# Kernel tuning notes

Measured on AMD Instinct MI355X. Metric: run time of the kernel, lower is better.

## Reference

```python
import jax, jax.numpy as jnp
import numpy as np
import math

# dims: batch, in-channels, freq bins, frames(=cropsize), ffn dim, bands
B, C, BINS, W, FF, NB = 16, 8, 1024, 256, 2048, 4
EPS = 1e-5


def _ln(x, g, b):
    m = x.mean(-1, keepdims=True)
    v = ((x - m) ** 2).mean(-1, keepdims=True)
    return (x - m) / jnp.sqrt(v + EPS) * g + b


def _conv1d(x, w, groups=1):
    # x: [b, Cin, L], w: [Cout, Cin//groups, K], 'same' padding
    pad = (w.shape[-1] - 1) // 2
    return jax.lax.conv_general_dilated(
        x, w, (1,), [(pad, pad)],
        dimension_numbers=('NCH', 'OIH', 'NCH'), feature_group_count=groups)


def _mb_attn(x, mem, qw, qb, kw, kb, vw, vb, ow, ob, er, dist_w):
    # MultibandFrameAttention with skewed relative-position bias
    b, w, c = x.shape
    d = c // NB
    q = (x @ qw.T + qb).reshape(b, w, NB, d).transpose(0, 2, 1, 3)    # [b,nb,w,d]
    k = (mem @ kw.T + kb).reshape(b, w, NB, d).transpose(0, 2, 3, 1)  # [b,nb,d,w]
    v = (mem @ vw.T + vb).reshape(b, w, NB, d).transpose(0, 2, 1, 3)  # [b,nb,w,d]
    # skew trick: q @ er -> pad left on last dim -> transpose -> drop first row
    qer = jnp.einsum('bnwd,dc->bnwc', q, er)                           # [b,nb,w,W]
    skew = jnp.pad(qer, ((0, 0), (0, 0), (0, 0), (1, 0)))
    skew = skew.transpose(0, 1, 3, 2)[:, :, 1:, :]                     # [b,nb,W,w]
    idx = jnp.arange(w)
    dist = jnp.abs(idx[:, None] - idx[None, :]).astype(x.dtype) / 2.0  # [w,w]
    p = dist[None] * dist_w + skew                                     # [b,nb,w,w]
    qk = jnp.einsum('bnwd,bndk->bnwk', q, k) / math.sqrt(c)
    a = jax.nn.softmax(qk + p, axis=-1)
    o = jnp.einsum('bnwk,bnkd->bnwd', a, v).transpose(0, 2, 1, 3).reshape(b, w, c)
    return o @ ow.T + ob


def setup_inputs() -> dict:
    key = jax.random.key(0)
    ks = jax.random.split(key, 24)
    rn = lambda k, s, sc=0.02: jax.random.normal(k, s, dtype=jnp.float32) * sc
    d = BINS // NB
    ones = lambda n: jnp.ones((n,), jnp.float32)
    zeros = lambda n: jnp.zeros((n,), jnp.float32)
    return {
        'x': jax.random.normal(ks[0], (B, C, BINS, W), jnp.float32),
        'bott_w': rn(ks[1], (1, C), 0.3),
        'bn_g': ones(1), 'bn_b': zeros(1), 'bn_m': zeros(1), 'bn_v': ones(1),
        'glu_w': rn(ks[2], (2 * BINS, BINS)),
        'n1g': ones(BINS), 'n1b': zeros(BINS),
        'c1L_w': rn(ks[3], (2 * FF, BINS)),
        'c1R_w': rn(ks[4], (FF // 2, BINS, 3)),
        'n2g': ones(2 * FF), 'n2b': zeros(2 * FF),
        'c2dw_w': rn(ks[5], (2 * FF, 1, 9), 0.1),
        'c2pw_w': rn(ks[6], (FF // 2, 2 * FF)),
        'n3g': ones(BINS), 'n3b': zeros(BINS),
        'qw': rn(ks[7], (BINS, BINS)), 'qb': zeros(BINS),
        'kw': rn(ks[8], (BINS, BINS)), 'kb': zeros(BINS),
        'vw': rn(ks[9], (BINS, BINS)), 'vb': zeros(BINS),
        'ow': rn(ks[10], (BINS, BINS)), 'ob': zeros(BINS),
        'er': rn(ks[11], (d, W), 0.02),
        'dist_w': rn(ks[12], (NB, W, 1), 0.02),
        'n4g': ones(BINS), 'n4b': zeros(BINS),
        'c3_w': rn(ks[13], (2 * FF, BINS)),
        'c4_w': rn(ks[14], (BINS, 2 * FF)),
        'n5g': ones(BINS), 'n5b': zeros(BINS),
    }


def reference(x, bott_w, bn_g, bn_b, bn_m, bn_v, glu_w, n1g, n1b,
              c1L_w, c1R_w, n2g, n2b, c2dw_w, c2pw_w, n3g, n3b,
              qw, qb, kw, kb, vw, vb, ow, ob, er, dist_w,
              n4g, n4b, c3_w, c4_w, n5g, n5b):
    # bottleneck: Linear(C->1) over channel dim, BatchNorm2d(1) eval, ReLU
    h0 = jnp.einsum('bchw,oc->bohw', x, bott_w)                        # [b,1,bins,w]
    h0 = (h0 - bn_m[None, :, None, None]) / jnp.sqrt(bn_v[None, :, None, None] + EPS)
    h0 = jax.nn.relu(h0 * bn_g[None, :, None, None] + bn_b[None, :, None, None])
    xs = h0[:, 0].transpose(0, 2, 1)                                   # [b,w,bins]

    # GLU block
    g = xs @ glu_w.T
    a, bgate = g[..., :BINS], g[..., BINS:]
    xs = _ln(xs + a * jax.nn.sigmoid(bgate), n1g, n1b)

    # conv/linear FFN
    hL = jax.nn.relu(xs @ c1L_w.T)                                     # [b,w,2ff]
    hR = jax.nn.relu(_conv1d(xs.transpose(0, 2, 1), c1R_w).transpose(0, 2, 1))
    hR = jnp.pad(hR, ((0, 0), (0, 0), (0, hL.shape[2] - hR.shape[2])))
    h = _ln(hL + hR, n2g, n2b)
    t = _conv1d(h.transpose(0, 2, 1), c2dw_w, groups=2 * FF)           # depthwise
    t = jnp.einsum('bcl,oc->bol', t, c2pw_w).transpose(0, 2, 1)        # [b,w,ff//2]
    t = jnp.pad(t, ((0, 0), (0, 0), (0, xs.shape[2] - t.shape[2])))
    xs = _ln(xs + t, n3g, n3b)

    # multiband attention (self)
    h = _mb_attn(xs, xs, qw, qb, kw, kb, vw, vb, ow, ob, er, dist_w)
    xs = _ln(xs + h, n4g, n4b)

    # final FFN
    h = jax.nn.relu(xs @ c3_w.T) @ c4_w.T
    xs = _ln(xs + h, n5g, n5b)
    return xs.transpose(0, 2, 1)[:, None]                              # [b,1,bins,w]
```

## Files before the change

### kernel.cpp

```cpp
#include <hip/hip_runtime.h>
#include <hip/hip_bf16.h>

#define EPSF 1e-5f

typedef unsigned short u16;
typedef unsigned int   u32;
typedef __attribute__((ext_vector_type(8))) short bf16x8;
typedef __attribute__((ext_vector_type(4))) float f32x4;

#define SWZ(row) (((row) & 7) << 3)

__device__ __forceinline__ u16 f2bf(float f) {
    u32 u = __builtin_bit_cast(u32, f);
    u32 r = u + 0x7fffu + ((u >> 16) & 1u);
    return (u16)(r >> 16);
}
__device__ __forceinline__ float bf2f(u16 h) {
    return __builtin_bit_cast(float, (u32)h << 16);
}
__device__ __forceinline__ float4 bf4f(ushort4 v) {
    return make_float4(bf2f(v.x), bf2f(v.y), bf2f(v.z), bf2f(v.w));
}
__device__ __forceinline__ ushort4 f4bf(float a, float b, float c, float d) {
    ushort4 o; o.x = f2bf(a); o.y = f2bf(b); o.z = f2bf(c); o.w = f2bf(d); return o;
}
__device__ __forceinline__ void gld16(void* lds, const void* gsrc) {
    __builtin_amdgcn_global_load_lds(
        (const __attribute__((address_space(1))) u32*)gsrc,
        (__attribute__((address_space(3))) u32*)lds, 16, 0, 0);
}

__device__ __forceinline__ float wred_sum(float v) {
#pragma unroll
    for (int off = 32; off; off >>= 1) v += __shfl_xor(v, off, 64);
    return v;
}
__device__ __forceinline__ void block_red2(float& s1, float& s2, int tid) {
    __shared__ float red[8];
    s1 = wred_sum(s1); s2 = wred_sum(s2);
    const int lane = tid & 63, wid = tid >> 6;
    if (!lane) { red[wid] = s1; red[4 + wid] = s2; }
    __syncthreads();
    s1 = red[0] + red[1] + red[2] + red[3];
    s2 = red[4] + red[5] + red[6] + red[7];
}

struct SetupArgs {
    const float* ws[9]; u16* wd[9]; int wn[9];
    const float* c1r; u16* c1rd;
    const float* er;  u16* erd;
    const float* dw;  float* dwd;
    const float* qb;  const float* kb; const float* vb; float* bcat;
    u16* zp;
    int off[15];
};
__global__ __launch_bounds__(256)
void setup_k(SetupArgs a)
{
    const int b = blockIdx.x;
    int seg = 0;
    while (seg < 13 && b >= a.off[seg + 1]) ++seg;
    const int i = (b - a.off[seg]) * 256 + threadIdx.x;
    if (seg < 9) {
        if (i < a.wn[seg]) {
            const float4 v = ((const float4*)a.ws[seg])[i];
            const float s = (seg == 6) ? 0.03125f : 1.f;
            ((ushort4*)a.wd[seg])[i] = f4bf(v.x * s, v.y * s, v.z * s, v.w * s);
        }
    } else if (seg == 9) {
        if (i < 3145728) {
            const int q = i / 3072, rem = i - q * 3072;
            const int ks = rem >> 10, ci = rem & 1023;
            a.c1rd[i] = f2bf(a.c1r[((long)q * 1024 + ci) * 3 + ks]);
        }
    } else if (seg == 10) {
        if (i < 65536) { const int c = i >> 8, d = i & 255; a.erd[i] = f2bf(a.er[d * 256 + c]); }
    } else if (seg == 11) {
        if (i < 36864) { const int k = i >> 12, c = i & 4095; a.dwd[i] = a.dw[c * 9 + k]; }
    } else if (seg == 12) {
        if (i < 3072) {
            const float* s = (i < 1024) ? a.qb : ((i < 2048) ? a.kb : a.vb);
            float v = s[i & 1023];
            if (i >= 1024 && i < 2048) v *= 0.03125f;
            a.bcat[i] = v;
        }
    } else {
        if (i < 8192) a.zp[i] = 0;
    }
}

__global__ __launch_bounds__(256)
void bottleneck_k(const float* __restrict__ x, const float* __restrict__ bw,
                  const float* __restrict__ bn_g, const float* __restrict__ bn_b,
                  const float* __restrict__ bn_m, const float* __restrict__ bn_v,
                  u16* __restrict__ xsb)
{
    __shared__ float tile[32][33];
    const int b = blockIdx.z, h0 = blockIdx.y * 32, w0 = blockIdx.x * 32;
    const int tid = threadIdx.x;
    const int tw = tid & 7, th = tid >> 3;
    float wreg[8];
#pragma unroll
    for (int ch = 0; ch < 8; ++ch) wreg[ch] = bw[ch];
    const float sc = bn_g[0] * rsqrtf(bn_v[0] + EPSF);
    const float sh = bn_b[0] - bn_m[0] * sc;
    float4 acc = make_float4(0.f, 0.f, 0.f, 0.f);
#pragma unroll
    for (int ch = 0; ch < 8; ++ch) {
        const float4 v = *(const float4*)&x[(((long)b * 8 + ch) * 1024 + h0 + th) * 256 + w0 + tw * 4];
        acc.x += v.x * wreg[ch]; acc.y += v.y * wreg[ch];
        acc.z += v.z * wreg[ch]; acc.w += v.w * wreg[ch];
    }
    tile[th][tw * 4 + 0] = fmaxf(acc.x * sc + sh, 0.f);
    tile[th][tw * 4 + 1] = fmaxf(acc.y * sc + sh, 0.f);
    tile[th][tw * 4 + 2] = fmaxf(acc.z * sc + sh, 0.f);
    tile[th][tw * 4 + 3] = fmaxf(acc.w * sc + sh, 0.f);
    __syncthreads();
    const int c = tid & 31, r = tid >> 5;
#pragma unroll
    for (int it = 0; it < 4; ++it) {
        const int wl = r + it * 8;
        xsb[((long)b * 256 + w0 + wl) * 1024 + h0 + c] = f2bf(tile[c][wl]);
    }
}

template<int ACT, int OUTBF, int BIAS, int SPLITK, int VOUT>
__global__ __launch_bounds__(512, 2)
void gemm8_k(const u16* __restrict__ A, const u16* __restrict__ B,
             const float* __restrict__ bias, void* __restrict__ Cout,
             int N, int K , int lda, int ldb, long partStride,
             u16* __restrict__ Vtp)
{
    extern __shared__ u16 lds[];
    const int m0 = blockIdx.y * 256, n0 = blockIdx.x * 256;
    const int koff = (SPLITK > 1) ? blockIdx.z * K : 0;
    const int nt = K >> 6;
    const int tid = threadIdx.x;
    const int lane = tid & 63, wid = tid >> 6;
    const int wr = ((wid >> 2) & 1) * 128;
    const int wc = (wid & 3) * 64;
    const int l15 = lane & 15, l4 = lane >> 4;

    const u16* Ag = A + (long)m0 * lda + koff;
    const u16* Bg = B + (long)n0 * ldb + koff;

    auto stage = [&](const u16* g, int ld, int ldsbase, int kcol, int h) {
#pragma unroll
        for (int is = 0; is < 2; ++is) {
            const int r = h * 128 + is * 64 + (tid >> 3);
            const int sc = ((tid & 7) * 8) ^ SWZ(r);
            gld16(&lds[ldsbase + h * 8192 + is * 4096 + tid * 8],
                  g + (long)r * ld + kcol + sc);
        }
    };
    auto frag = [&](int base, int row, int col) -> bf16x8 {
        return *(const bf16x8*)&lds[base + row * 64 + (col ^ SWZ(row))];
    };

    f32x4 acc[8][4] = {};

    stage(Ag, lda, 0, 0, 0);
    stage(Ag, lda, 0, 0, 1);
    stage(Bg, ldb, 32768, 0, 0);
    stage(Bg, ldb, 32768, 0, 1);
    if (nt > 1) {
        stage(Bg, ldb, 49152, 64, 0);
        stage(Bg, ldb, 49152, 64, 1);
        stage(Ag, lda, 16384, 64, 0);
        asm volatile("s_waitcnt vmcnt(6)" ::: "memory");
    } else {
        asm volatile("s_waitcnt vmcnt(0)" ::: "memory");
    }
    __builtin_amdgcn_s_barrier();

    for (int kt = 0; kt < nt; ++kt) {
        const int cs = kt & 1;
        const int ab = cs * 16384;
        const int bb = 32768 + cs * 16384;
        const int abn = (cs ^ 1) * 16384;
        const int kc1 = (kt + 1) * 64, kc2 = (kt + 2) * 64;
        bf16x8 alo[4][2], ahi[4][2], b01[2][2], b23[2][2];

#pragma unroll
        for (int i = 0; i < 4; ++i)
#pragma unroll
            for (int kk = 0; kk < 2; ++kk)
                alo[i][kk] = frag(ab, wr + i * 16 + l15, kk * 32 + l4 * 8);
#pragma unroll
        for (int j = 0; j < 2; ++j)
#pragma unroll
            for (int kk = 0; kk < 2; ++kk)
                b01[j][kk] = frag(bb, wc + j * 16 + l15, kk * 32 + l4 * 8);
        if (kt + 1 < nt) stage(Ag, lda, abn, kc1, 1);
        __builtin_amdgcn_s_barrier();
        asm volatile("s_waitcnt lgkmcnt(0)" ::: "memory");
        __builtin_amdgcn_s_setprio(1);
#pragma unroll
        for (int i = 0; i < 4; ++i)
#pragma unroll
            for (int j = 0; j < 2; ++j)
#pragma unroll
                for (int kk = 0; kk < 2; ++kk)
                    acc[i][j] = __builtin_amdgcn_mfma_f32_16x16x32_bf16(alo[i][kk], b01[j][kk], acc[i][j], 0, 0, 0);
        __builtin_amdgcn_s_setprio(0);
        __builtin_amdgcn_s_barrier();

#pragma unroll
        for (int j = 0; j < 2; ++j)
#pragma unroll
            for (int kk = 0; kk < 2; ++kk)
                b23[j][kk] = frag(bb, wc + (j + 2) * 16 + l15, kk * 32 + l4 * 8);
        if (kt + 2 < nt) stage(Bg, ldb, bb, kc2, 0);
        __builtin_amdgcn_s_barrier();
        asm volatile("s_waitcnt lgkmcnt(0)" ::: "memory");
        __builtin_amdgcn_s_setprio(1);
#pragma unroll
        for (int i = 0; i < 4; ++i)
#pragma unroll
            for (int j = 0; j < 2; ++j)
#pragma unroll
                for (int kk = 0; kk < 2; ++kk)
                    acc[i][j + 2] = __builtin_amdgcn_mfma_f32_16x16x32_bf16(alo[i][kk], b23[j][kk], acc[i][j + 2], 0, 0, 0);
        __builtin_amdgcn_s_setprio(0);
        __builtin_amdgcn_s_barrier();

#pragma unroll
        for (int i = 0; i < 4; ++i)
#pragma unroll
            for (int kk = 0; kk < 2; ++kk)
                ahi[i][kk] = frag(ab, wr + (i + 4) * 16 + l15, kk * 32 + l4 * 8);
        if (kt + 2 < nt) stage(Bg, ldb, bb, kc2, 1);
        __builtin_amdgcn_s_barrier();
        asm volatile("s_waitcnt lgkmcnt(0)" ::: "memory");
        __builtin_amdgcn_s_setprio(1);
#pragma unroll
        for (int i = 0; i < 4; ++i)
#pragma unroll
            for (int j = 0; j < 2; ++j)
#pragma unroll
                for (int kk = 0; kk < 2; ++kk)
                    acc[i + 4][j + 2] = __builtin_amdgcn_mfma_f32_16x16x32_bf16(ahi[i][kk], b23[j][kk], acc[i + 4][j + 2], 0, 0, 0);
        __builtin_amdgcn_s_setprio(0);
        __builtin_amdgcn_s_barrier();

        if (kt + 2 < nt) stage(Ag, lda, ab, kc2, 0);
        __builtin_amdgcn_s_barrier();
        __builtin_amdgcn_s_setprio(1);
#pragma unroll
        for (int i = 0; i < 4; ++i)
#pragma unroll
            for (int j = 0; j < 2; ++j)
#pragma unroll
                for (int kk = 0; kk < 2; ++kk)
                    acc[i + 4][j] = __builtin_amdgcn_mfma_f32_16x16x32_bf16(ahi[i][kk], b01[j][kk], acc[i + 4][j], 0, 0, 0);
        __builtin_amdgcn_s_setprio(0);
        if (kt + 2 < nt) {
            asm volatile("s_waitcnt vmcnt(6)" ::: "memory");
        } else {
            asm volatile("s_waitcnt vmcnt(0)" ::: "memory");
        }
        __builtin_amdgcn_s_barrier();
    }

    if (VOUT && n0 >= 2048) {
        const int zb4 = (m0 >> 8) * 4;
#pragma unroll
        for (int i = 0; i < 8; ++i)
#pragma unroll
            for (int j = 0; j < 4; ++j) {
                const int n = n0 + wc + j * 16 + l15;
                const int d = n - 2048, zn = d >> 8, dl = d & 255;
                const float bv = BIAS ? bias[n] : 0.f;
                const int w = wr + i * 16 + l4 * 4;
                ushort4 st = f4bf(acc[i][j][0] + bv, acc[i][j][1] + bv,
                                  acc[i][j][2] + bv, acc[i][j][3] + bv);
                *(ushort4*)&Vtp[((long)(zb4 + zn) * 256 + dl) * 256 + w] = st;
            }
    } else if (SPLITK > 1) {
        u16* Cp = (u16*)Cout + (long)blockIdx.z * partStride;
#pragma unroll
        for (int i = 0; i < 8; ++i)
#pragma unroll
            for (int j = 0; j < 4; ++j) {
                const int n = n0 + wc + j * 16 + l15;
#pragma unroll
                for (int q = 0; q < 4; ++q) {
                    const int m = m0 + wr + i * 16 + l4 * 4 + q;
                    Cp[(long)m * N + n] = f2bf(acc[i][j][q]);
                }
            }
    } else {
        float* Cf = (float*)Cout;
        u16*   Cb = (u16*)Cout;
#pragma unroll
        for (int i = 0; i < 8; ++i)
#pragma unroll
            for (int j = 0; j < 4; ++j) {
                const int n = n0 + wc + j * 16 + l15;
                const float bv = BIAS ? bias[n] : 0.f;
#pragma unroll
                for (int q = 0; q < 4; ++q) {
                    const int m = m0 + wr + i * 16 + l4 * 4 + q;
                    float v = acc[i][j][q] + bv;
                    if (ACT) v = fmaxf(v, 0.f);
                    if (OUTBF) Cb[(long)m * N + n] = f2bf(v);
                    else       Cf[(long)m * N + n] = v;
                }
            }
    }
}

__global__ __launch_bounds__(512, 2)
void ffconv8_k(const u16* __restrict__ Xb, const u16* __restrict__ Wl,
               const u16* __restrict__ Wr, const u16* __restrict__ zp,
               u16* __restrict__ Hout, u16* __restrict__ Cp3)
{
    extern __shared__ u16 lds[];
    const int bx = blockIdx.x;
    const int m0 = blockIdx.y * 256;
    const bool conv = bx >= 16;
    const int tap  = conv ? ((bx - 16) >> 2) : 0;
    const int shift = conv ? (tap - 1) : 0;
    const int n0 = conv ? (((bx - 16) & 3) * 256) : (bx * 256);
    const u16* Bbase = conv ? (Wr + (long)n0 * 3072 + tap * 1024)
                            : (Wl + (long)n0 * 1024);
    const int ldb = conv ? 3072 : 1024;
    const int nt = 16;
    const int tid = threadIdx.x;
    const int lane = tid & 63, wid = tid >> 6;
    const int wr = ((wid >> 2) & 1) * 128;
    const int wc = (wid & 3) * 64;
    const int l15 = lane & 15, l4 = lane >> 4;

    auto stageA = [&](int ldsbase, int kcol, int h) {
#pragma unroll
        for (int is = 0; is < 2; ++is) {
            const int r = h * 128 + is * 64 + (tid >> 3);
            const int sc = ((tid & 7) * 8) ^ SWZ(r);
            const int t = m0 + r;
            const int wp = (t & 255) + shift;
            const u16* src = ((unsigned)wp < 256u)
                ? Xb + (long)(t + shift) * 1024 + kcol + sc
                : zp;
            gld16(&lds[ldsbase + h * 8192 + is * 4096 + tid * 8], src);
        }
    };
    auto stageB = [&](int ldsbase, int kcol, int h) {
#pragma unroll
        for (int is = 0; is < 2; ++is) {
            const int r = h * 128 + is * 64 + (tid >> 3);
            const int sc = ((tid & 7) * 8) ^ SWZ(r);
            gld16(&lds[ldsbase + h * 8192 + is * 4096 + tid * 8],
                  Bbase + (long)r * ldb + kcol + sc);
        }
    };
    auto frag = [&](int base, int row, int col) -> bf16x8 {
        return *(const bf16x8*)&lds[base + row * 64 + (col ^ SWZ(row))];
    };

    f32x4 acc[8][4] = {};

    stageA(0, 0, 0);
    stageA(0, 0, 1);
    stageB(32768, 0, 0);
    stageB(32768, 0, 1);
    stageB(49152, 64, 0);
    stageB(49152, 64, 1);
    stageA(16384, 64, 0);
    asm volatile("s_waitcnt vmcnt(6)" ::: "memory");
    __builtin_amdgcn_s_barrier();

    for (int kt = 0; kt < nt; ++kt) {
        const int cs = kt & 1;
        const int ab = cs * 16384;
        const int bb = 32768 + cs * 16384;
        const int abn = (cs ^ 1) * 16384;
        const int kc1 = (kt + 1) * 64, kc2 = (kt + 2) * 64;
        bf16x8 alo[4][2], ahi[4][2], b01[2][2], b23[2][2];

#pragma unroll
        for (int i = 0; i < 4; ++i)
#pragma unroll
            for (int kk = 0; kk < 2; ++kk)
                alo[i][kk] = frag(ab, wr + i * 16 + l15, kk * 32 + l4 * 8);
#pragma unroll
        for (int j = 0; j < 2; ++j)
#pragma unroll
            for (int kk = 0; kk < 2; ++kk)
                b01[j][kk] = frag(bb, wc + j * 16 + l15, kk * 32 + l4 * 8);
        if (kt + 1 < nt) stageA(abn, kc1, 1);
        __builtin_amdgcn_s_barrier();
        asm volatile("s_waitcnt lgkmcnt(0)" ::: "memory");
        __builtin_amdgcn_s_setprio(1);
#pragma unroll
        for (int i = 0; i < 4; ++i)
#pragma unroll
            for (int j = 0; j < 2; ++j)
#pragma unroll
                for (int kk = 0; kk < 2; ++kk)
                    acc[i][j] = __builtin_amdgcn_mfma_f32_16x16x32_bf16(alo[i][kk], b01[j][kk], acc[i][j], 0, 0, 0);
        __builtin_amdgcn_s_setprio(0);
        __builtin_amdgcn_s_barrier();

#pragma unroll
        for (int j = 0; j < 2; ++j)
#pragma unroll
            for (int kk = 0; kk < 2; ++kk)
                b23[j][kk] = frag(bb, wc + (j + 2) * 16 + l15, kk * 32 + l4 * 8);
        if (kt + 2 < nt) stageB(bb, kc2, 0);
        __builtin_amdgcn_s_barrier();
        asm volatile("s_waitcnt lgkmcnt(0)" ::: "memory");
        __builtin_amdgcn_s_setprio(1);
#pragma unroll
        for (int i = 0; i < 4; ++i)
#pragma unroll
            for (int j = 0; j < 2; ++j)
#pragma unroll
                for (int kk = 0; kk < 2; ++kk)
                    acc[i][j + 2] = __builtin_amdgcn_mfma_f32_16x16x32_bf16(alo[i][kk], b23[j][kk], acc[i][j + 2], 0, 0, 0);
        __builtin_amdgcn_s_setprio(0);
        __builtin_amdgcn_s_barrier();

#pragma unroll
        for (int i = 0; i < 4; ++i)
#pragma unroll
            for (int kk = 0; kk < 2; ++kk)
                ahi[i][kk] = frag(ab, wr + (i + 4) * 16 + l15, kk * 32 + l4 * 8);
        if (kt + 2 < nt) stageB(bb, kc2, 1);
        __builtin_amdgcn_s_barrier();
        asm volatile("s_waitcnt lgkmcnt(0)" ::: "memory");
        __builtin_amdgcn_s_setprio(1);
#pragma unroll
        for (int i = 0; i < 4; ++i)
#pragma unroll
            for (int j = 0; j < 2; ++j)
#pragma unroll
                for (int kk = 0; kk < 2; ++kk)
                    acc[i + 4][j + 2] = __builtin_amdgcn_mfma_f32_16x16x32_bf16(ahi[i][kk], b23[j][kk], acc[i + 4][j + 2], 0, 0, 0);
        __builtin_amdgcn_s_setprio(0);
        __builtin_amdgcn_s_barrier();

        if (kt + 2 < nt) stageA(ab, kc2, 0);
        __builtin_amdgcn_s_barrier();
        __builtin_amdgcn_s_setprio(1);
#pragma unroll
        for (int i = 0; i < 4; ++i)
#pragma unroll
            for (int j = 0; j < 2; ++j)
#pragma unroll
                for (int kk = 0; kk < 2; ++kk)
                    acc[i + 4][j] = __builtin_amdgcn_mfma_f32_16x16x32_bf16(ahi[i][kk], b01[j][kk], acc[i + 4][j], 0, 0, 0);
        __builtin_amdgcn_s_setprio(0);
        if (kt + 2 < nt) {
            asm volatile("s_waitcnt vmcnt(6)" ::: "memory");
        } else {
            asm volatile("s_waitcnt vmcnt(0)" ::: "memory");
        }
        __builtin_amdgcn_s_barrier();
    }

    if (conv) {
        u16* Cp = Cp3 + (long)tap * 4194304;
#pragma unroll
        for (int i = 0; i < 8; ++i)
#pragma unroll
            for (int j = 0; j < 4; ++j) {
                const int n = n0 + wc + j * 16 + l15;
#pragma unroll
                for (int q = 0; q < 4; ++q) {
                    const int m = m0 + wr + i * 16 + l4 * 4 + q;
                    Cp[(long)m * 1024 + n] = f2bf(acc[i][j][q]);
                }
            }
    } else {
#pragma unroll
        for (int i = 0; i < 8; ++i)
#pragma unroll
            for (int j = 0; j < 4; ++j) {
                const int n = n0 + wc + j * 16 + l15;
#pragma unroll
                for (int q = 0; q < 4; ++q) {
                    const int m = m0 + wr + i * 16 + l4 * 4 + q;
                    Hout[(long)m * 4096 + n] = f2bf(fmaxf(acc[i][j][q], 0.f));
                }
            }
    }
}

__global__ __launch_bounds__(256, 2)
void attn_fused_k(const u16* __restrict__ QKVb, const u16* __restrict__ erT,
                  const u16* __restrict__ Vt, const float* __restrict__ dwp,
                  u16* __restrict__ Oc)
{
    __shared__ __align__(16) u16 As[4096];
    __shared__ __align__(16) u16 Bs[16384];
    __shared__ __align__(16) u16 Pl[16384];
    __shared__ float redM[4][64];
    __shared__ float redS[4][64];
    const int z = blockIdx.y, zb = z >> 2, zn = z & 3;
    const int m0 = blockIdx.x * 64;
    const int tid = threadIdx.x;
    const int lane = tid & 63, wid = tid >> 6;
    const int l15 = lane & 15, l4 = lane >> 4;

    const u16* Qg = QKVb + (long)(zb * 256) * 3072 + zn * 256;
    const u16* Kg = Qg + 1024;

    auto stageA64 = [&](const u16* g, long ld) {
#pragma unroll
        for (int p = 0; p < 2; ++p) {
            const int e = p * 2048 + tid * 8;
            const int r = e >> 6, c = e & 63;
            const int sc = c ^ SWZ(r);
            gld16(&As[e], g + (long)r * ld + sc);
        }
    };
    auto stageB256 = [&](const u16* g, long ld) {
#pragma unroll
        for (int p = 0; p < 8; ++p) {
            const int e = p * 2048 + tid * 8;
            const int r = e >> 6, c = e & 63;
            const int sc = c ^ SWZ(r);
            gld16(&Bs[e], g + (long)r * ld + sc);
        }
    };
    auto fragA = [&](int i, int kk) -> bf16x8 {
        const int row = i * 16 + l15, col = kk * 32 + l4 * 8;
        return *(const bf16x8*)&As[row * 64 + (col ^ SWZ(row))];
    };
    auto fragB = [&](int j, int kk) -> bf16x8 {
        const int row = wid * 64 + j * 16 + l15, col = kk * 32 + l4 * 8;
        return *(const bf16x8*)&Bs[row * 64 + (col ^ SWZ(row))];
    };
    auto fragP = [&](int kc, int i, int kk) -> bf16x8 {
        const int row = i * 16 + l15, col = kk * 32 + l4 * 8;
        return *(const bf16x8*)&Pl[kc * 4096 + row * 64 + (col ^ SWZ(row))];
    };

    f32x4 acc1[4][4] = {};

    for (int kc = 0; kc < 8; ++kc) {
        __syncthreads();
        if (kc < 4) {
            stageA64(Qg + (long)m0 * 3072 + kc * 64, 3072);
            stageB256(Kg + kc * 64, 3072);
        } else {
            stageA64(erT + (long)m0 * 256 + (kc - 4) * 64, 256);
            stageB256(Qg + (kc - 4) * 64, 3072);
        }
        __syncthreads();
#pragma unroll
        for (int i = 0; i < 4; ++i) {
            const bf16x8 a0 = fragA(i, 0), a1 = fragA(i, 1);
#pragma unroll
            for (int j = 0; j < 4; ++j) {
                acc1[i][j] = __builtin_amdgcn_mfma_f32_16x16x32_bf16(a0, fragB(j, 0), acc1[i][j], 0, 0, 0);
                acc1[i][j] = __builtin_amdgcn_mfma_f32_16x16x32_bf16(a1, fragB(j, 1), acc1[i][j], 0, 0, 0);
            }
        }
    }

#pragma unroll
    for (int i = 0; i < 4; ++i)
#pragma unroll
        for (int q = 0; q < 4; ++q) {
            const int mg = m0 + i * 16 + l4 * 4 + q;
            const float dw = dwp[zn * 256 + mg];
#pragma unroll
            for (int j = 0; j < 4; ++j) {
                const int ng = wid * 64 + j * 16 + l15;
                acc1[i][j][q] += fabsf((float)(mg - ng)) * 0.5f * dw;
            }
        }

    float rmax[4][4], rsum[4][4];
#pragma unroll
    for (int i = 0; i < 4; ++i)
#pragma unroll
        for (int q = 0; q < 4; ++q) {
            float mv = fmaxf(fmaxf(acc1[i][0][q], acc1[i][1][q]),
                             fmaxf(acc1[i][2][q], acc1[i][3][q]));
#pragma unroll
            for (int off = 1; off <= 8; off <<= 1) mv = fmaxf(mv, __shfl_xor(mv, off, 64));
            rmax[i][q] = mv;
        }
    if (l15 == 0) {
#pragma unroll
        for (int i = 0; i < 4; ++i)
#pragma unroll
            for (int q = 0; q < 4; ++q)
                redM[wid][i * 16 + l4 * 4 + q] = rmax[i][q];
    }
    __syncthreads();
#pragma unroll
    for (int i = 0; i < 4; ++i)
#pragma unroll
        for (int q = 0; q < 4; ++q) {
            const int ml = i * 16 + l4 * 4 + q;
            rmax[i][q] = fmaxf(fmaxf(redM[0][ml], redM[1][ml]), fmaxf(redM[2][ml], redM[3][ml]));
        }
#pragma unroll
    for (int i = 0; i < 4; ++i)
#pragma unroll
        for (int q = 0; q < 4; ++q) {
            float sv = 0.f;
#pragma unroll
            for (int j = 0; j < 4; ++j) {
                const float e = __expf(acc1[i][j][q] - rmax[i][q]);
                acc1[i][j][q] = e;
                sv += e;
            }
#pragma unroll
            for (int off = 1; off <= 8; off <<= 1) sv += __shfl_xor(sv, off, 64);
            rsum[i][q] = sv;
        }
    if (l15 == 0) {
#pragma unroll
        for (int i = 0; i < 4; ++i)
#pragma unroll
            for (int q = 0; q < 4; ++q)
                redS[wid][i * 16 + l4 * 4 + q] = rsum[i][q];
    }
    __syncthreads();
#pragma unroll
    for (int i = 0; i < 4; ++i)
#pragma unroll
        for (int q = 0; q < 4; ++q) {
            const int ml = i * 16 + l4 * 4 + q;
            rsum[i][q] = redS[0][ml] + redS[1][ml] + redS[2][ml] + redS[3][ml];
        }
#pragma unroll
    for (int i = 0; i < 4; ++i)
#pragma unroll
        for (int q = 0; q < 4; ++q) {
            const float rinv = 1.f / rsum[i][q];
            const int ml = i * 16 + l4 * 4 + q;
#pragma unroll
            for (int j = 0; j < 4; ++j) {
                const int nc = j * 16 + l15;
                Pl[wid * 4096 + ml * 64 + (nc ^ SWZ(ml))] = f2bf(acc1[i][j][q] * rinv);
            }
        }
    __syncthreads();

    f32x4 accO[4][4] = {};
    for (int kc = 0; kc < 4; ++kc) {
        __syncthreads();
        stageB256(Vt + (long)(z * 256) * 256 + kc * 64, 256);
        __syncthreads();
#pragma unroll
        for (int i = 0; i < 4; ++i) {
            const bf16x8 a0 = fragP(kc, i, 0), a1 = fragP(kc, i, 1);
#pragma unroll
            for (int j = 0; j < 4; ++j) {
                accO[i][j] = __builtin_amdgcn_mfma_f32_16x16x32_bf16(a0, fragB(j, 0), accO[i][j], 0, 0, 0);
                accO[i][j] = __builtin_amdgcn_mfma_f32_16x16x32_bf16(a1, fragB(j, 1), accO[i][j], 0, 0, 0);
            }
        }
    }

#pragma unroll
    for (int i = 0; i < 4; ++i)
#pragma unroll
        for (int j = 0; j < 4; ++j) {
            const int d = wid * 64 + j * 16 + l15;
#pragma unroll
            for (int q = 0; q < 4; ++q) {
                const int mg = m0 + i * 16 + l4 * 4 + q;
                Oc[(long)(zb * 256 + mg) * 1024 + zn * 256 + d] = f2bf(accO[i][j][q]);
            }
        }
}

__global__ __launch_bounds__(256)
void glu_ln_k(const u16* __restrict__ xs0, const u16* __restrict__ g2,
              const float* __restrict__ gam, const float* __restrict__ bet,
              u16* __restrict__ outb)
{
    const int t = blockIdx.x, tid = threadIdx.x;
    const int f0 = tid * 4;
    const long PS = 8388608;
    const float4 xv = bf4f(*(const ushort4*)&xs0[(long)t * 1024 + f0]);
    const float4 a0 = bf4f(*(const ushort4*)&g2[(long)t * 2048 + f0]);
    const float4 g0 = bf4f(*(const ushort4*)&g2[(long)t * 2048 + 1024 + f0]);
    const float4 a1 = bf4f(*(const ushort4*)&g2[PS + (long)t * 2048 + f0]);
    const float4 g1 = bf4f(*(const ushort4*)&g2[PS + (long)t * 2048 + 1024 + f0]);
    const float ax = a0.x + a1.x, ay = a0.y + a1.y, az = a0.z + a1.z, aw = a0.w + a1.w;
    const float gx = g0.x + g1.x, gy = g0.y + g1.y, gz = g0.z + g1.z, gw = g0.w + g1.w;
    float vals[4];
    vals[0] = xv.x + ax / (1.f + expf(-gx));
    vals[1] = xv.y + ay / (1.f + expf(-gy));
    vals[2] = xv.z + az / (1.f + expf(-gz));
    vals[3] = xv.w + aw / (1.f + expf(-gw));
    float s1 = vals[0] + vals[1] + vals[2] + vals[3];
    float s2 = vals[0]*vals[0] + vals[1]*vals[1] + vals[2]*vals[2] + vals[3]*vals[3];
    block_red2(s1, s2, tid);
    const float mean = s1 * (1.f / 1024.f);
    const float var  = s2 * (1.f / 1024.f) - mean * mean;
    const float rstd = rsqrtf(var + EPSF);
    const float4 gm = *(const float4*)&gam[f0];
    const float4 bt = *(const float4*)&bet[f0];
    *(ushort4*)&outb[(long)t * 1024 + f0] = f4bf(
        (vals[0] - mean) * rstd * gm.x + bt.x,
        (vals[1] - mean) * rstd * gm.y + bt.y,
        (vals[2] - mean) * rstd * gm.z + bt.z,
        (vals[3] - mean) * rstd * gm.w + bt.w);
}

template<int P, int BIAS>
__global__ __launch_bounds__(256)
void add_ln1024_k(const u16* __restrict__ A, const u16* __restrict__ Bp,
                  const float* __restrict__ bias,
                  const float* __restrict__ gam, const float* __restrict__ bet,
                  u16* __restrict__ outb)
{
    const int t = blockIdx.x, tid = threadIdx.x;
    const int f0 = tid * 4;
    const long PS = 4194304;
    const float4 a = bf4f(*(const ushort4*)&A[(long)t * 1024 + f0]);
    float4 b = bf4f(*(const ushort4*)&Bp[(long)t * 1024 + f0]);
#pragma unroll
    for (int p = 1; p < P; ++p) {
        const float4 bp = bf4f(*(const ushort4*)&Bp[p * PS + (long)t * 1024 + f0]);
        b.x += bp.x; b.y += bp.y; b.z += bp.z; b.w += bp.w;
    }
    if (BIAS) {
        const float4 bb = *(const float4*)&bias[f0];
        b.x += bb.x; b.y += bb.y; b.z += bb.z; b.w += bb.w;
    }
    float vals[4] = {a.x + b.x, a.y + b.y, a.z + b.z, a.w + b.w};
    float s1 = vals[0] + vals[1] + vals[2] + vals[3];
    float s2 = vals[0]*vals[0] + vals[1]*vals[1] + vals[2]*vals[2] + vals[3]*vals[3];
    block_red2(s1, s2, tid);
    const float mean = s1 * (1.f / 1024.f);
    const float var  = s2 * (1.f / 1024.f) - mean * mean;
    const float rstd = rsqrtf(var + EPSF);
    const float4 gm = *(const float4*)&gam[f0];
    const float4 bt = *(const float4*)&bet[f0];
    *(ushort4*)&outb[(long)t * 1024 + f0] = f4bf(
        (vals[0] - mean) * rstd * gm.x + bt.x,
        (vals[1] - mean) * rstd * gm.y + bt.y,
        (vals[2] - mean) * rstd * gm.z + bt.z,
        (vals[3] - mean) * rstd * gm.w + bt.w);
}

__global__ __launch_bounds__(256)
void add_ln4096_k(const u16* __restrict__ A, const u16* __restrict__ Bp,
                  const float* __restrict__ gam, const float* __restrict__ bet,
                  u16* __restrict__ outb)
{
    const int t = blockIdx.x, tid = threadIdx.x;
    const long PS = 4194304;
    const int f0 = tid * 16;
    float vals[16];
    const bf16x8 a0 = *(const bf16x8*)&A[(long)t * 4096 + f0];
    const bf16x8 a1 = *(const bf16x8*)&A[(long)t * 4096 + f0 + 8];
#pragma unroll
    for (int e = 0; e < 8; ++e) { vals[e] = bf2f((u16)a0[e]); vals[8 + e] = bf2f((u16)a1[e]); }
    if (tid < 64) {
#pragma unroll
        for (int c = 0; c < 4; ++c) {
            const int fc = f0 + c * 4;
            const float4 b0 = bf4f(*(const ushort4*)&Bp[(long)t * 1024 + fc]);
            const float4 b1 = bf4f(*(const ushort4*)&Bp[PS + (long)t * 1024 + fc]);
            const float4 b2 = bf4f(*(const ushort4*)&Bp[2 * PS + (long)t * 1024 + fc]);
            vals[c*4+0] += fmaxf(b0.x + b1.x + b2.x, 0.f);
            vals[c*4+1] += fmaxf(b0.y + b1.y + b2.y, 0.f);
            vals[c*4+2] += fmaxf(b0.z + b1.z + b2.z, 0.f);
            vals[c*4+3] += fmaxf(b0.w + b1.w + b2.w, 0.f);
        }
    }
    float s1 = 0.f, s2 = 0.f;
#pragma unroll
    for (int e = 0; e < 16; ++e) { s1 += vals[e]; s2 += vals[e] * vals[e]; }
    block_red2(s1, s2, tid);
    const float mean = s1 * (1.f / 4096.f);
    const float var  = s2 * (1.f / 4096.f) - mean * mean;
    const float rstd = rsqrtf(var + EPSF);
#pragma unroll
    for (int c = 0; c < 4; ++c) {
        const int fc = f0 + c * 4;
        const float4 gm = *(const float4*)&gam[fc];
        const float4 bt = *(const float4*)&bet[fc];
        *(ushort4*)&outb[(long)t * 4096 + fc] = f4bf(
            (vals[c*4+0] - mean) * rstd * gm.x + bt.x,
            (vals[c*4+1] - mean) * rstd * gm.y + bt.y,
            (vals[c*4+2] - mean) * rstd * gm.z + bt.z,
            (vals[c*4+3] - mean) * rstd * gm.w + bt.w);
    }
}

__global__ __launch_bounds__(256)
void dwconv8_k(const u16* __restrict__ h, const float* __restrict__ wT,
               u16* __restrict__ out)
{
    const long idx = (long)blockIdx.x * 256 + threadIdx.x;
    const int cg = (int)(idx & 511);
    const int t  = (int)(idx >> 9);
    const int w  = t & 255;
    const int c0 = cg * 8;
    float acc[8] = {};
#pragma unroll
    for (int k = 0; k < 9; ++k) {
        const int wp = w + k - 4;
        if ((unsigned)wp < 256u) {
            const bf16x8 hv = *(const bf16x8*)&h[(long)(t + k - 4) * 4096 + c0];
            const float4 w0 = *(const float4*)&wT[k * 4096 + c0];
            const float4 w1 = *(const float4*)&wT[k * 4096 + c0 + 4];
            acc[0] += bf2f((u16)hv[0]) * w0.x;
            acc[1] += bf2f((u16)hv[1]) * w0.y;
            acc[2] += bf2f((u16)hv[2]) * w0.z;
            acc[3] += bf2f((u16)hv[3]) * w0.w;
            acc[4] += bf2f((u16)hv[4]) * w1.x;
            acc[5] += bf2f((u16)hv[5]) * w1.y;
            acc[6] += bf2f((u16)hv[6]) * w1.z;
            acc[7] += bf2f((u16)hv[7]) * w1.w;
        }
    }
    bf16x8 res;
#pragma unroll
    for (int j = 0; j < 8; ++j) res[j] = (short)f2bf(acc[j]);
    *(bf16x8*)&out[(long)t * 4096 + c0] = res;
}

__global__ __launch_bounds__(256)
void transpose_out_k(const u16* __restrict__ xs, float* __restrict__ out)
{
    __shared__ u16 tile[32][34];
    const int b = blockIdx.z, f0 = blockIdx.y * 32, w0 = blockIdx.x * 32;
    const int tid = threadIdx.x, c = tid & 31, r = tid >> 5;
#pragma unroll
    for (int it = 0; it < 4; ++it) {
        const int w = w0 + r + it * 8;
        tile[r + it * 8][c] = xs[((long)b * 256 + w) * 1024 + f0 + c];
    }
    __syncthreads();
#pragma unroll
    for (int it = 0; it < 4; ++it) {
        const int fl = r + it * 8;
        out[((long)b * 1024 + f0 + fl) * 256 + w0 + c] = bf2f(tile[c][fl]);
    }
}

extern "C" void kernel_launch(void* const* d_in, const int* in_sizes, int n_in,
                              void* d_out, int out_size, void* d_ws, size_t ws_size,
                              hipStream_t stream)
{
    const float* x      = (const float*)d_in[0];
    const float* bott_w = (const float*)d_in[1];
    const float* bn_g   = (const float*)d_in[2];
    const float* bn_b   = (const float*)d_in[3];
    const float* bn_m   = (const float*)d_in[4];
    const float* bn_v   = (const float*)d_in[5];
    const float* glu_w  = (const float*)d_in[6];
    const float* n1g    = (const float*)d_in[7];
    const float* n1b    = (const float*)d_in[8];
    const float* c1L_w  = (const float*)d_in[9];
    const float* c1R_w  = (const float*)d_in[10];
    const float* n2g    = (const float*)d_in[11];
    const float* n2b    = (const float*)d_in[12];
    const float* c2dw_w = (const float*)d_in[13];
    const float* c2pw_w = (const float*)d_in[14];
    const float* n3g    = (const float*)d_in[15];
    const float* n3b    = (const float*)d_in[16];
    const float* qw     = (const float*)d_in[17];
    const float* qb     = (const float*)d_in[18];
    const float* kw     = (const float*)d_in[19];
    const float* kb     = (const float*)d_in[20];
    const float* vw     = (const float*)d_in[21];
    const float* vb     = (const float*)d_in[22];
    const float* ow     = (const float*)d_in[23];
    const float* ob     = (const float*)d_in[24];
    const float* er     = (const float*)d_in[25];
    const float* dist_w = (const float*)d_in[26];
    const float* n4g    = (const float*)d_in[27];
    const float* n4b    = (const float*)d_in[28];
    const float* c3_w   = (const float*)d_in[29];
    const float* c4_w   = (const float*)d_in[30];
    const float* n5g    = (const float*)d_in[31];
    const float* n5b    = (const float*)d_in[32];
    float* out = (float*)d_out;

    char* Wb_ = (char*)d_ws;
    auto Bf = [&](size_t mib) { return (u16*)(Wb_ + (mib << 20)); };
    u16* XA   = Bf(0);
    u16* XB   = Bf(8);
    u16* H0b  = Bf(32);
    u16* Hglu = Bf(64);
    u16* C3p  = Bf(64);
    u16* P4   = Bf(64);
    u16* H1b  = Bf(128);
    u16* Hdw  = Bf(160);
    u16* QKVb = Bf(192);
    u16* Vt   = Bf(216);
    u16* S1b  = Bf(264);
    u16* wGLU = Bf(296); u16* wC1L = Bf(300); u16* wC1R = Bf(308);
    u16* wC2P = Bf(314); u16* wQKV = Bf(322); u16* wO   = Bf(328);
    u16* wC3  = Bf(330); u16* wC4  = Bf(338);
    u16* erT  = Bf(346);
    u16* zp   = (u16*)(Wb_ + (346u << 20) + 131072);
    float* wdwT = (float*)(Wb_ + (346u << 20) + 131072 + 16384);
    float* bQKV = (float*)(Wb_ + (346u << 20) + 131072 + 16384 + 147456);

    const dim3 blk(256);
    const dim3 blk8(512);
    const long PS1 = 4194304;
    const size_t SH8 = 131072;

    SetupArgs sa;
    sa.ws[0] = glu_w;  sa.wd[0] = wGLU;            sa.wn[0] = 524288;
    sa.ws[1] = c1L_w;  sa.wd[1] = wC1L;            sa.wn[1] = 1048576;
    sa.ws[2] = c2pw_w; sa.wd[2] = wC2P;            sa.wn[2] = 1048576;
    sa.ws[3] = c3_w;   sa.wd[3] = wC3;             sa.wn[3] = 1048576;
    sa.ws[4] = c4_w;   sa.wd[4] = wC4;             sa.wn[4] = 1048576;
    sa.ws[5] = qw;     sa.wd[5] = wQKV;            sa.wn[5] = 262144;
    sa.ws[6] = kw;     sa.wd[6] = wQKV + 1048576;  sa.wn[6] = 262144;
    sa.ws[7] = vw;     sa.wd[7] = wQKV + 2097152;  sa.wn[7] = 262144;
    sa.ws[8] = ow;     sa.wd[8] = wO;              sa.wn[8] = 262144;
    sa.c1r = c1R_w; sa.c1rd = wC1R;
    sa.er  = er;    sa.erd  = erT;
    sa.dw  = c2dw_w; sa.dwd = wdwT;
    sa.qb = qb; sa.kb = kb; sa.vb = vb; sa.bcat = bQKV;
    sa.zp = zp;
    {
        int bc[14] = {2048, 4096, 4096, 4096, 4096, 1024, 1024, 1024, 1024,
                      12288, 256, 144, 12, 32};
        int acc = 0;
        for (int s = 0; s < 14; ++s) { sa.off[s] = acc; acc += bc[s]; }
        sa.off[14] = acc;
        setup_k<<<dim3(acc), blk, 0, stream>>>(sa);
    }

    bottleneck_k<<<dim3(8, 32, 16), blk, 0, stream>>>(x, bott_w, bn_g, bn_b, bn_m, bn_v, XA);

    gemm8_k<0,0,0,2,0><<<dim3(8, 16, 2), blk8, SH8, stream>>>(XA, wGLU, nullptr, Hglu,
        2048, 512, 1024, 1024, (long)4096 * 2048, nullptr);

    glu_ln_k<<<dim3(4096), blk, 0, stream>>>(XA, Hglu, n1g, n1b, XB);

    ffconv8_k<<<dim3(28, 16), blk8, SH8, stream>>>(XB, wC1L, wC1R, zp, H0b, C3p);

    add_ln4096_k<<<dim3(4096), blk, 0, stream>>>(H0b, C3p, n2g, n2b, H1b);

    dwconv8_k<<<dim3(8192), blk, 0, stream>>>(H1b, wdwT, Hdw);

    gemm8_k<0,0,0,4,0><<<dim3(4, 16, 4), blk8, SH8, stream>>>(Hdw, wC2P, nullptr, P4,
        1024, 1024, 4096, 4096, PS1, nullptr);

    add_ln1024_k<4,0><<<dim3(4096), blk, 0, stream>>>(XB, P4, nullptr, n3g, n3b, XA);

    gemm8_k<0,1,1,1,1><<<dim3(12, 16, 1), blk8, SH8, stream>>>(XA, wQKV, bQKV, QKVb,
        3072, 1024, 1024, 1024, 0, Vt);

    attn_fused_k<<<dim3(4, 64), blk, 0, stream>>>(QKVb, erT, Vt, dist_w, S1b);

    gemm8_k<0,0,0,4,0><<<dim3(4, 16, 4), blk8, SH8, stream>>>(S1b, wO, nullptr, P4,
        1024, 256, 1024, 1024, PS1, nullptr);

    add_ln1024_k<4,1><<<dim3(4096), blk, 0, stream>>>(XA, P4, ob, n4g, n4b, XB);

    gemm8_k<1,1,0,1,0><<<dim3(16, 16, 1), blk8, SH8, stream>>>(XB, wC3, nullptr, H0b,
        4096, 1024, 1024, 1024, 0, nullptr);

    gemm8_k<0,0,0,4,0><<<dim3(4, 16, 4), blk8, SH8, stream>>>(H0b, wC4, nullptr, P4,
        1024, 1024, 4096, 4096, PS1, nullptr);

    add_ln1024_k<4,0><<<dim3(4096), blk, 0, stream>>>(XB, P4, nullptr, n5g, n5b, XA);

    transpose_out_k<<<dim3(8, 32, 16), blk, 0, stream>>>(XA, out);

    (void)in_sizes; (void)n_in; (void)out_size; (void)ws_size;
}
```

Measured before the change: 464.6 us.

## Accumulate all three conv taps in-kernel instead of split-K partials

The conv branch of the fused FFN GEMM kernel now loops over all three taps inside one block (K=3072), rather than launching separate blocks per tap that write three partial outputs. ReLU is applied in the epilogue and a single bf16 buffer is written, so the add+LN kernel reads one buffer instead of three. This removes two partial-buffer writes and reads, but the grid shrinks from 448 to 320 blocks, and the conv blocks do three times the K work, which may lengthen the tail.

```diff
diff --git a/kernel.cpp b/kernel.cpp
--- a/kernel.cpp
+++ b/kernel.cpp
@@ -313,19 +313,16 @@
 __global__ __launch_bounds__(512, 2)
 void ffconv8_k(const u16* __restrict__ Xb, const u16* __restrict__ Wl,
                const u16* __restrict__ Wr, const u16* __restrict__ zp,
-               u16* __restrict__ Hout, u16* __restrict__ Cp3)
+               u16* __restrict__ Hout, u16* __restrict__ C3s)
 {
     extern __shared__ u16 lds[];
     const int bx = blockIdx.x;
     const int m0 = blockIdx.y * 256;
     const bool conv = bx >= 16;
-    const int tap  = conv ? ((bx - 16) >> 2) : 0;
-    const int shift = conv ? (tap - 1) : 0;
-    const int n0 = conv ? (((bx - 16) & 3) * 256) : (bx * 256);
-    const u16* Bbase = conv ? (Wr + (long)n0 * 3072 + tap * 1024)
-                            : (Wl + (long)n0 * 1024);
+    const int n0 = conv ? ((bx - 16) * 256) : (bx * 256);
+    const u16* Bbase = conv ? (Wr + (long)n0 * 3072) : (Wl + (long)n0 * 1024);
     const int ldb = conv ? 3072 : 1024;
-    const int nt = 16;
+    const int nt = conv ? 48 : 16;
     const int tid = threadIdx.x;
     const int lane = tid & 63, wid = tid >> 6;
     const int wr = ((wid >> 2) & 1) * 128;
@@ -333,6 +330,8 @@
     const int l15 = lane & 15, l4 = lane >> 4;
 
     auto stageA = [&](int ldsbase, int kcol, int h) {
+        const int shift = conv ? ((kcol >> 10) - 1) : 0;
+        const int ci = conv ? (kcol & 1023) : kcol;
 #pragma unroll
         for (int is = 0; is < 2; ++is) {
             const int r = h * 128 + is * 64 + (tid >> 3);
@@ -340,7 +339,7 @@
             const int t = m0 + r;
             const int wp = (t & 255) + shift;
             const u16* src = ((unsigned)wp < 256u)
-                ? Xb + (long)(t + shift) * 1024 + kcol + sc
+                ? Xb + (long)(t + shift) * 1024 + ci + sc
                 : zp;
             gld16(&lds[ldsbase + h * 8192 + is * 4096 + tid * 8], src);
         }
@@ -460,7 +459,6 @@
     }
 
     if (conv) {
-        u16* Cp = Cp3 + (long)tap * 4194304;
 #pragma unroll
         for (int i = 0; i < 8; ++i)
 #pragma unroll
@@ -469,7 +467,7 @@
 #pragma unroll
                 for (int q = 0; q < 4; ++q) {
                     const int m = m0 + wr + i * 16 + l4 * 4 + q;
-                    Cp[(long)m * 1024 + n] = f2bf(acc[i][j][q]);
+                    C3s[(long)m * 1024 + n] = f2bf(fmaxf(acc[i][j][q], 0.f));
                 }
             }
     } else {
@@ -745,12 +743,11 @@
 }
 
 __global__ __launch_bounds__(256)
-void add_ln4096_k(const u16* __restrict__ A, const u16* __restrict__ Bp,
+void add_ln4096_k(const u16* __restrict__ A, const u16* __restrict__ C3,
                   const float* __restrict__ gam, const float* __restrict__ bet,
                   u16* __restrict__ outb)
 {
     const int t = blockIdx.x, tid = threadIdx.x;
-    const long PS = 4194304;
     const int f0 = tid * 16;
     float vals[16];
     const bf16x8 a0 = *(const bf16x8*)&A[(long)t * 4096 + f0];
@@ -758,17 +755,10 @@
 #pragma unroll
     for (int e = 0; e < 8; ++e) { vals[e] = bf2f((u16)a0[e]); vals[8 + e] = bf2f((u16)a1[e]); }
     if (tid < 64) {
-#pragma unroll
-        for (int c = 0; c < 4; ++c) {
-            const int fc = f0 + c * 4;
-            const float4 b0 = bf4f(*(const ushort4*)&Bp[(long)t * 1024 + fc]);
-            const float4 b1 = bf4f(*(const ushort4*)&Bp[PS + (long)t * 1024 + fc]);
-            const float4 b2 = bf4f(*(const ushort4*)&Bp[2 * PS + (long)t * 1024 + fc]);
-            vals[c*4+0] += fmaxf(b0.x + b1.x + b2.x, 0.f);
-            vals[c*4+1] += fmaxf(b0.y + b1.y + b2.y, 0.f);
-            vals[c*4+2] += fmaxf(b0.z + b1.z + b2.z, 0.f);
-            vals[c*4+3] += fmaxf(b0.w + b1.w + b2.w, 0.f);
-        }
+        const bf16x8 b0 = *(const bf16x8*)&C3[(long)t * 1024 + f0];
+        const bf16x8 b1 = *(const bf16x8*)&C3[(long)t * 1024 + f0 + 8];
+#pragma unroll
+        for (int e = 0; e < 8; ++e) { vals[e] += bf2f((u16)b0[e]); vals[8 + e] += bf2f((u16)b1[e]); }
     }
     float s1 = 0.f, s2 = 0.f;
 #pragma unroll
@@ -887,7 +877,7 @@
     u16* XB   = Bf(8);
     u16* H0b  = Bf(32);
     u16* Hglu = Bf(64);
-    u16* C3p  = Bf(64);
+    u16* C3s  = Bf(64);
     u16* P4   = Bf(64);
     u16* H1b  = Bf(128);
     u16* Hdw  = Bf(160);
@@ -938,9 +928,9 @@
 
     glu_ln_k<<<dim3(4096), blk, 0, stream>>>(XA, Hglu, n1g, n1b, XB);
 
-    ffconv8_k<<<dim3(28, 16), blk8, SH8, stream>>>(XB, wC1L, wC1R, zp, H0b, C3p);
-
-    add_ln4096_k<<<dim3(4096), blk, 0, stream>>>(H0b, C3p, n2g, n2b, H1b);
+    ffconv8_k<<<dim3(20, 16), blk8, SH8, stream>>>(XB, wC1L, wC1R, zp, H0b, C3s);
+
+    add_ln4096_k<<<dim3(4096), blk, 0, stream>>>(H0b, C3s, n2g, n2b, H1b);
 
     dwconv8_k<<<dim3(8192), blk, 0, stream>>>(H1b, wdwT, Hdw);
 
```

New measurement: 512.2 us. 10.2% more time.
